# Optimization experiments

Hardware: AMD Instinct MI355X
Metric: run time of the kernel (lower is better)

Reference implementation:

```python
import jax, jax.numpy as jnp
import numpy as np

EPS = 1e-8

def prelu(x, a):
    return jnp.where(x >= 0, x, a * x)

def setup_inputs() -> dict:
    key = jax.random.key(0)
    ks = jax.random.split(key, 8)
    B, G, N, T = 4, 8, 128, 6000
    H = 384
    x = jax.random.normal(ks[0], (B, G, N, T), dtype=jnp.float32)
    # torch.nn.Linear default init: U(-1/sqrt(fan_in), 1/sqrt(fan_in))
    def lin(k, out_f, in_f):
        k1, k2 = jax.random.split(k)
        bound = 1.0 / np.sqrt(in_f)
        W = jax.random.uniform(k1, (out_f, in_f), minval=-bound, maxval=bound, dtype=jnp.float32)
        b = jax.random.uniform(k2, (out_f,), minval=-bound, maxval=bound, dtype=jnp.float32)
        return W, b
    Wi, bi = lin(ks[1], H, N)
    Wm, bm = lin(ks[2], H, H)
    Wo, bo = lin(ks[3], N, 2 * H)
    # PReLU default: single learnable scalar initialized to 0.25
    ai = jnp.float32(0.25)
    am = jnp.float32(0.25)
    ao = jnp.float32(0.25)
    gamma = jnp.ones((N,), dtype=jnp.float32)
    beta = jnp.zeros((N,), dtype=jnp.float32)
    return {"input": x, "Wi": Wi, "bi": bi, "ai": ai, "Wm": Wm, "bm": bm, "am": am,
            "Wo": Wo, "bo": bo, "ao": ao, "gamma": gamma, "beta": beta}

def reference(input, Wi, bi, ai, Wm, bm, am, Wo, bo, ao, gamma, beta):
    B, G, N, T = input.shape
    # [B, T, G, N]
    h = jnp.transpose(input, (0, 3, 1, 2))
    # TAC_input: Linear(N->H) + PReLU
    gi = prelu(jnp.einsum('btgn,hn->btgh', h, Wi) + bi, ai)          # [B,T,G,H]
    # mean over groups, TAC_mean: Linear(H->H) + PReLU
    gm = gi.mean(axis=2)                                              # [B,T,H]
    gm = prelu(jnp.einsum('bth,oh->bto', gm, Wm) + bm, am)            # [B,T,H]
    gm = jnp.broadcast_to(gm[:, :, None, :], gi.shape)                # [B,T,G,H]
    cat = jnp.concatenate([gi, gm], axis=-1)                          # [B,T,G,2H]
    # TAC_output: Linear(2H->N) + PReLU
    go = prelu(jnp.einsum('btgc,nc->btgn', cat, Wo) + bo, ao)         # [B,T,G,N]
    go = jnp.transpose(go, (0, 2, 3, 1))                              # [B,G,N,T]
    # GlobLN over (N, T) per (batch*G) sample, affine along channel N
    mean = go.mean(axis=(2, 3), keepdims=True)
    var = jnp.mean((go - mean) ** 2, axis=(2, 3), keepdims=True)
    normed = (go - mean) / jnp.sqrt(var + EPS)
    go = gamma[None, None, :, None] * normed + beta[None, None, :, None]
    return input + go
```

## Files before the change

kernel.cpp:

```cpp
#include <hip/hip_runtime.h>

typedef __bf16 bf16_t;
typedef __bf16 bf16x8 __attribute__((ext_vector_type(8)));
typedef float f32x4 __attribute__((ext_vector_type(4)));

static constexpr int Bq = 4, Gg = 8, Nn = 128, Tt = 6000, Hh = 384;
static constexpr int TB = 16;
static constexpr int NTPB = Tt / TB;
static constexpr int NTILES = Bq * NTPB;
static constexpr int LDA = 136;
static constexpr int LDG = 392;
static constexpr int LDSM = 392;
static constexpr int LDV = 132;

static constexpr size_t OFF_WI  = 0;
static constexpr size_t OFF_WM  = OFF_WI + (size_t)Hh * Nn * 2;
static constexpr size_t OFF_WO  = OFF_WM + (size_t)Hh * Hh * 2;
static constexpr size_t OFF_PT  = OFF_WO + (size_t)Nn * 2 * Hh * 2;
static constexpr size_t OFF_MRS = OFF_PT + (size_t)NTILES * 8 * 16 * 4;
static constexpr size_t OFF_GO  = (size_t)2 << 20;
static constexpr size_t WS_NEED = OFF_GO + (size_t)Bq * Tt * Gg * Nn * 2;

static constexpr int SM_GI = 0;
static constexpr int SM_SM = 100352;
static constexpr int SM_AS = 112896;
static constexpr int SM_MM = 112896;
static constexpr int SM_VV = 112896 + 12544;
static constexpr int SMEM_BYTES = 147712;

#define MFMA16(a, b, c) __builtin_amdgcn_mfma_f32_16x16x32_bf16((a), (b), (c), 0, 0, 0)

__global__ void k0_prep(const float* __restrict__ Wi, const float* __restrict__ Wm,
                        const float* __restrict__ Wo,
                        bf16_t* __restrict__ WiB, bf16_t* __restrict__ WmB,
                        bf16_t* __restrict__ WoB) {
    int i = blockIdx.x * blockDim.x + threadIdx.x;
    const int n1 = Hh * Nn, n2 = Hh * Hh, n3 = Nn * 2 * Hh;
    for (int idx = i; idx < n1 + n2 + n3; idx += gridDim.x * blockDim.x) {
        if (idx < n1)            WiB[idx] = (bf16_t)Wi[idx];
        else if (idx < n1 + n2)  WmB[idx - n1] = (bf16_t)Wm[idx - n1];
        else                     WoB[idx - n1 - n2] = (bf16_t)Wo[idx - n1 - n2];
    }
}

__device__ __forceinline__ int as_col(int row, int c) {
    return ((((c >> 3) ^ ((row >> 3) & 7)) << 3) | (c & 7));
}

__global__ __launch_bounds__(512, 1)
void k1_fused(const float* __restrict__ x,
              const bf16_t* __restrict__ WiB, const float* __restrict__ bi, const float* __restrict__ aip,
              const bf16_t* __restrict__ WmB, const float* __restrict__ bm, const float* __restrict__ amp,
              const bf16_t* __restrict__ WoB, const float* __restrict__ bo, const float* __restrict__ aop,
              bf16_t* __restrict__ go, float* __restrict__ part) {
    __shared__ char smem[SMEM_BYTES];
    bf16_t* Gi = (bf16_t*)(smem + SM_GI);
    bf16_t* Sm = (bf16_t*)(smem + SM_SM);
    bf16_t* As = (bf16_t*)(smem + SM_AS);
    bf16_t* Mm = (bf16_t*)(smem + SM_MM);
    float*  Vv = (float*)(smem + SM_VV);

    const int tid  = threadIdx.x;
    const int lane = tid & 63;
    const int w    = tid >> 6;
    const int l15  = lane & 15;
    const int l4   = lane >> 4;
    const int tile = blockIdx.x;
    const int b    = tile / NTPB, t0 = (tile % NTPB) * TB;

    {
        const int g0 = tid >> 7, n0 = tid & 127;
        #pragma unroll
        for (int h = 0; h < 2; h++) {
            int gg = g0 + 4 * h;
            #pragma unroll
            for (int q = 0; q < 4; q++) {
                f32x4 xv = *(const f32x4*)&x[((size_t)((b * Gg + gg) * Nn + n0)) * Tt + t0 + 4 * q];
                #pragma unroll
                for (int e = 0; e < 4; e++) {
                    int row = (q * 4 + e) * Gg + gg;
                    As[row * LDA + as_col(row, n0)] = (bf16_t)xv[e];
                }
            }
        }
    }
    __syncthreads();

    const float ai = aip[0], am = amp[0], ao = aop[0];

    {
        const int cb = w * 48;
        f32x4 acc[8][3];
        #pragma unroll
        for (int mt = 0; mt < 8; mt++)
            #pragma unroll
            for (int nc = 0; nc < 3; nc++) acc[mt][nc] = f32x4{0.f, 0.f, 0.f, 0.f};
        #pragma unroll
        for (int kk = 0; kk < 4; kk++) {
            const int k0 = kk * 32 + l4 * 8;
            bf16x8 bb[3];
            #pragma unroll
            for (int nc = 0; nc < 3; nc++)
                bb[nc] = *(const bf16x8*)&WiB[(cb + nc * 16 + l15) * Nn + k0];
            #pragma unroll
            for (int mt = 0; mt < 8; mt++) {
                int row = mt * 16 + l15;
                bf16x8 a = *(const bf16x8*)&As[row * LDA + as_col(row, k0)];
                #pragma unroll
                for (int nc = 0; nc < 3; nc++) acc[mt][nc] = MFMA16(a, bb[nc], acc[mt][nc]);
            }
        }
        #pragma unroll
        for (int nc = 0; nc < 3; nc++) {
            int col = cb + nc * 16 + l15;
            float bv = bi[col];
            #pragma unroll
            for (int mt = 0; mt < 8; mt++) {
                float ms = 0.f;
                #pragma unroll
                for (int j = 0; j < 4; j++) {
                    int row = mt * 16 + l4 * 4 + j;
                    float v = acc[mt][nc][j] + bv;
                    v = v >= 0.f ? v : ai * v;
                    Gi[row * LDG + col] = (bf16_t)v;
                    ms += v;
                }
                ms += __shfl_xor(ms, 16, 64);
                if ((l4 & 1) == 0) {
                    int tl = mt * 2 + (l4 >> 1);
                    Sm[tl * LDSM + col] = (bf16_t)(0.125f * ms);
                }
            }
        }
    }
    __syncthreads();

    {
        const int cb2 = w * 48;
        f32x4 acc2[3];
        #pragma unroll
        for (int nc = 0; nc < 3; nc++) acc2[nc] = f32x4{0.f, 0.f, 0.f, 0.f};
        #pragma unroll
        for (int kk = 0; kk < 12; kk++) {
            const int k0 = kk * 32 + l4 * 8;
            bf16x8 a = *(const bf16x8*)&Sm[l15 * LDSM + k0];
            #pragma unroll
            for (int nc = 0; nc < 3; nc++) {
                bf16x8 bb = *(const bf16x8*)&WmB[(cb2 + nc * 16 + l15) * Hh + k0];
                acc2[nc] = MFMA16(a, bb, acc2[nc]);
            }
        }
        #pragma unroll
        for (int nc = 0; nc < 3; nc++) {
            int col = cb2 + nc * 16 + l15;
            float bv = bm[col];
            #pragma unroll
            for (int j = 0; j < 4; j++) {
                float v = acc2[nc][j] + bv;
                v = v >= 0.f ? v : am * v;
                Mm[(l4 * 4 + j) * LDSM + col] = (bf16_t)v;
            }
        }
    }
    __syncthreads();

    {
        const int nblk = w * 16;
        f32x4 acc3 = f32x4{0.f, 0.f, 0.f, 0.f};
        #pragma unroll
        for (int kk = 0; kk < 12; kk++) {
            const int k0 = kk * 32 + l4 * 8;
            bf16x8 a = *(const bf16x8*)&Mm[l15 * LDSM + k0];
            bf16x8 bb = *(const bf16x8*)&WoB[(nblk + l15) * 768 + 384 + k0];
            acc3 = MFMA16(a, bb, acc3);
        }
        #pragma unroll
        for (int j = 0; j < 4; j++) Vv[(l4 * 4 + j) * LDV + nblk + l15] = acc3[j];
    }

    const int mh = w >> 2, ws4 = w & 3;
    const int cb4 = ws4 * 32;
    f32x4 acc4[4][2];
    #pragma unroll
    for (int mt = 0; mt < 4; mt++)
        #pragma unroll
        for (int nc = 0; nc < 2; nc++) acc4[mt][nc] = f32x4{0.f, 0.f, 0.f, 0.f};
    #pragma unroll
    for (int kk = 0; kk < 12; kk++) {
        const int k0 = kk * 32 + l4 * 8;
        bf16x8 b0 = *(const bf16x8*)&WoB[(cb4 + l15) * 768 + k0];
        bf16x8 b1 = *(const bf16x8*)&WoB[(cb4 + 16 + l15) * 768 + k0];
        bf16x8 a[4];
        #pragma unroll
        for (int mt = 0; mt < 4; mt++)
            a[mt] = *(const bf16x8*)&Gi[(mh * 64 + mt * 16 + l15) * LDG + k0];
        #pragma unroll
        for (int mt = 0; mt < 4; mt++) {
            acc4[mt][0] = MFMA16(a[mt], b0, acc4[mt][0]);
            acc4[mt][1] = MFMA16(a[mt], b1, acc4[mt][1]);
        }
    }
    __syncthreads();

    {
        float gsum[4] = {0.f, 0.f, 0.f, 0.f};
        float gss[4]  = {0.f, 0.f, 0.f, 0.f};
        #pragma unroll
        for (int nc = 0; nc < 2; nc++) {
            int col = cb4 + nc * 16 + l15;
            float bv = bo[col];
            #pragma unroll
            for (int mt = 0; mt < 4; mt++) {
                #pragma unroll
                for (int j = 0; j < 4; j++) {
                    int row = mh * 64 + mt * 16 + l4 * 4 + j;
                    int tl = row >> 3;
                    int g = row & 7;
                    float v = acc4[mt][nc][j] + Vv[tl * LDV + col] + bv;
                    v = v >= 0.f ? v : ao * v;
                    go[((size_t)((b * Tt + t0 + tl) * Gg + g)) * Nn + col] = (bf16_t)v;
                    gsum[j] += v;
                    gss[j] += v * v;
                }
            }
        }
        #pragma unroll
        for (int j = 0; j < 4; j++) {
            float s = gsum[j], q = gss[j];
            #pragma unroll
            for (int off = 1; off < 16; off <<= 1) {
                s += __shfl_xor(s, off, 64);
                q += __shfl_xor(q, off, 64);
            }
            s += __shfl_xor(s, 32, 64);
            q += __shfl_xor(q, 32, 64);
            if (l15 == 0 && l4 < 2) {
                int g = l4 * 4 + j;
                part[((size_t)tile * 8 + w) * 16 + g * 2 + 0] = s;
                part[((size_t)tile * 8 + w) * 16 + g * 2 + 1] = q;
            }
        }
    }
}

__global__ __launch_bounds__(1024)
void k_final(const float* __restrict__ part, float* __restrict__ mr) {
    __shared__ float red[64][17];
    const int tid = threadIdx.x, key = tid & 63, chunk = tid >> 6;
    const int bb = key >> 4;
    const int rowsPerB = NTPB * 8;
    const int t0 = chunk * 188;
    const int cnt = min(188, rowsPerB - t0);
    float s = 0.f;
    for (int i = 0; i < cnt; i++)
        s += part[(size_t)(bb * rowsPerB + t0 + i) * 16 + (key & 15)];
    red[key][chunk] = s;
    __syncthreads();
    if (tid < 64) {
        float tot = 0.f;
        #pragma unroll
        for (int ch = 0; ch < 16; ch++) tot += red[tid][ch];
        red[tid][16] = tot;
    }
    __syncthreads();
    if (tid < 32) {
        int b2 = tid >> 3, g2 = tid & 7;
        float s0 = red[b2 * 16 + g2 * 2][16];
        float s1 = red[b2 * 16 + g2 * 2 + 1][16];
        const float cntf = (float)Nn * (float)Tt;
        float mean = s0 / cntf;
        float var = s1 / cntf - mean * mean;
        mr[tid * 2] = mean;
        mr[tid * 2 + 1] = rsqrtf(var + 1e-8f);
    }
}

__global__ __launch_bounds__(256)
void k_apply(const float* __restrict__ x, const bf16_t* __restrict__ go,
             const float* __restrict__ mr, const float* __restrict__ gamma,
             const float* __restrict__ beta, float* __restrict__ out) {
    __shared__ float tr[32][65];
    int bid = blockIdx.x;
    const int tt = bid % 94; bid /= 94;
    const int nn = bid & 3;  bid >>= 2;
    const int g = bid & 7;
    const int b = bid >> 3;
    const int t0 = tt * 64, n0 = nn * 32;
    const int tid = threadIdx.x;
    const float mean = mr[(b * 8 + g) * 2], rstd = mr[(b * 8 + g) * 2 + 1];

    for (int idx = tid; idx < 2048; idx += 256) {
        int nl = idx & 31, tl = idx >> 5;
        int t = t0 + tl;
        float v = 0.f;
        if (t < Tt) v = (float)go[((size_t)((b * Tt + t) * Gg + g)) * Nn + n0 + nl];
        tr[nl][tl] = v;
    }
    __syncthreads();
    for (int idx = tid; idx < 2048; idx += 256) {
        int tl = idx & 63, nl = idx >> 6;
        int t = t0 + tl;
        if (t < Tt) {
            int n = n0 + nl;
            size_t a = ((size_t)((b * Gg + g) * Nn + n)) * Tt + t;
            out[a] = x[a] + gamma[n] * (tr[nl][tl] - mean) * rstd + beta[n];
        }
    }
}

extern "C" void kernel_launch(void* const* d_in, const int* in_sizes, int n_in,
                              void* d_out, int out_size, void* d_ws, size_t ws_size,
                              hipStream_t stream) {
    const float* x     = (const float*)d_in[0];
    const float* Wi    = (const float*)d_in[1];
    const float* bi    = (const float*)d_in[2];
    const float* ai    = (const float*)d_in[3];
    const float* Wm    = (const float*)d_in[4];
    const float* bm    = (const float*)d_in[5];
    const float* am    = (const float*)d_in[6];
    const float* Wo    = (const float*)d_in[7];
    const float* bo    = (const float*)d_in[8];
    const float* ao    = (const float*)d_in[9];
    const float* gamma = (const float*)d_in[10];
    const float* beta  = (const float*)d_in[11];
    float* out = (float*)d_out;
    char* ws = (char*)d_ws;

    if (ws_size < WS_NEED) return;

    bf16_t* WiB = (bf16_t*)(ws + OFF_WI);
    bf16_t* WmB = (bf16_t*)(ws + OFF_WM);
    bf16_t* WoB = (bf16_t*)(ws + OFF_WO);
    float*  prt = (float*)(ws + OFF_PT);
    float*  mrs = (float*)(ws + OFF_MRS);
    bf16_t* goB = (bf16_t*)(ws + OFF_GO);

    k0_prep<<<dim3(512), dim3(256), 0, stream>>>(Wi, Wm, Wo, WiB, WmB, WoB);
    k1_fused<<<dim3(NTILES), dim3(512), 0, stream>>>(
        x, WiB, bi, ai, WmB, bm, am, WoB, bo, ao, goB, prt);
    k_final<<<dim3(1), dim3(1024), 0, stream>>>(prt, mrs);
    k_apply<<<dim3(Bq * Gg * 4 * 94), dim3(256), 0, stream>>>(x, goB, mrs, gamma, beta, out);
}
```

Before: 294.5 us.

## Stage biases in LDS, nontemporal I/O, per-tile stat reduction via shared atomics

```diff
diff --git a/kernel.cpp b/kernel.cpp
--- a/kernel.cpp
+++ b/kernel.cpp
@@ -17,7 +17,7 @@
 static constexpr size_t OFF_WM  = OFF_WI + (size_t)Hh * Nn * 2;
 static constexpr size_t OFF_WO  = OFF_WM + (size_t)Hh * Hh * 2;
 static constexpr size_t OFF_PT  = OFF_WO + (size_t)Nn * 2 * Hh * 2;
-static constexpr size_t OFF_MRS = OFF_PT + (size_t)NTILES * 8 * 16 * 4;
+static constexpr size_t OFF_MRS = OFF_PT + (size_t)NTILES * 16 * 4;
 static constexpr size_t OFF_GO  = (size_t)2 << 20;
 static constexpr size_t WS_NEED = OFF_GO + (size_t)Bq * Tt * Gg * Nn * 2;
 
@@ -26,7 +26,11 @@
 static constexpr int SM_AS = 112896;
 static constexpr int SM_MM = 112896;
 static constexpr int SM_VV = 112896 + 12544;
-static constexpr int SMEM_BYTES = 147712;
+static constexpr int SM_BI = 147712;
+static constexpr int SM_BM = 149248;
+static constexpr int SM_BO = 150784;
+static constexpr int SM_ST = 151296;
+static constexpr int SMEM_BYTES = 151360;
 
 #define MFMA16(a, b, c) __builtin_amdgcn_mfma_f32_16x16x32_bf16((a), (b), (c), 0, 0, 0)
 
@@ -59,6 +63,10 @@
     bf16_t* As = (bf16_t*)(smem + SM_AS);
     bf16_t* Mm = (bf16_t*)(smem + SM_MM);
     float*  Vv = (float*)(smem + SM_VV);
+    float*  sbi = (float*)(smem + SM_BI);
+    float*  sbm = (float*)(smem + SM_BM);
+    float*  sbo = (float*)(smem + SM_BO);
+    float*  st  = (float*)(smem + SM_ST);
 
     const int tid  = threadIdx.x;
     const int lane = tid & 63;
@@ -68,6 +76,10 @@
     const int tile = blockIdx.x;
     const int b    = tile / NTPB, t0 = (tile % NTPB) * TB;
 
+    if (tid < 384) { sbi[tid] = bi[tid]; sbm[tid] = bm[tid]; }
+    if (tid >= 384 && tid < 512) sbo[tid - 384] = bo[tid - 384];
+    if (tid < 16) st[tid] = 0.f;
+
     {
         const int g0 = tid >> 7, n0 = tid & 127;
         #pragma unroll
@@ -75,7 +87,8 @@
             int gg = g0 + 4 * h;
             #pragma unroll
             for (int q = 0; q < 4; q++) {
-                f32x4 xv = *(const f32x4*)&x[((size_t)((b * Gg + gg) * Nn + n0)) * Tt + t0 + 4 * q];
+                f32x4 xv = __builtin_nontemporal_load(
+                    (const f32x4*)&x[((size_t)((b * Gg + gg) * Nn + n0)) * Tt + t0 + 4 * q]);
                 #pragma unroll
                 for (int e = 0; e < 4; e++) {
                     int row = (q * 4 + e) * Gg + gg;
@@ -113,7 +126,7 @@
         #pragma unroll
         for (int nc = 0; nc < 3; nc++) {
             int col = cb + nc * 16 + l15;
-            float bv = bi[col];
+            float bv = sbi[col];
             #pragma unroll
             for (int mt = 0; mt < 8; mt++) {
                 float ms = 0.f;
@@ -153,7 +166,7 @@
         #pragma unroll
         for (int nc = 0; nc < 3; nc++) {
             int col = cb2 + nc * 16 + l15;
-            float bv = bm[col];
+            float bv = sbm[col];
             #pragma unroll
             for (int j = 0; j < 4; j++) {
                 float v = acc2[nc][j] + bv;
@@ -208,7 +221,7 @@
         #pragma unroll
         for (int nc = 0; nc < 2; nc++) {
             int col = cb4 + nc * 16 + l15;
-            float bv = bo[col];
+            float bv = sbo[col];
             #pragma unroll
             for (int mt = 0; mt < 4; mt++) {
                 #pragma unroll
@@ -218,7 +231,8 @@
                     int g = row & 7;
                     float v = acc4[mt][nc][j] + Vv[tl * LDV + col] + bv;
                     v = v >= 0.f ? v : ao * v;
-                    go[((size_t)((b * Tt + t0 + tl) * Gg + g)) * Nn + col] = (bf16_t)v;
+                    __builtin_nontemporal_store(
+                        (bf16_t)v, &go[((size_t)((b * Tt + t0 + tl) * Gg + g)) * Nn + col]);
                     gsum[j] += v;
                     gss[j] += v * v;
                 }
@@ -236,37 +250,40 @@
             q += __shfl_xor(q, 32, 64);
             if (l15 == 0 && l4 < 2) {
                 int g = l4 * 4 + j;
-                part[((size_t)tile * 8 + w) * 16 + g * 2 + 0] = s;
-                part[((size_t)tile * 8 + w) * 16 + g * 2 + 1] = q;
-            }
-        }
-    }
+                atomicAdd(&st[g * 2 + 0], s);
+                atomicAdd(&st[g * 2 + 1], q);
+            }
+        }
+    }
+    __syncthreads();
+    if (tid < 16) part[(size_t)tile * 16 + tid] = st[tid];
 }
 
 __global__ __launch_bounds__(1024)
 void k_final(const float* __restrict__ part, float* __restrict__ mr) {
-    __shared__ float red[64][17];
-    const int tid = threadIdx.x, key = tid & 63, chunk = tid >> 6;
-    const int bb = key >> 4;
-    const int rowsPerB = NTPB * 8;
-    const int t0 = chunk * 188;
-    const int cnt = min(188, rowsPerB - t0);
-    float s = 0.f;
-    for (int i = 0; i < cnt; i++)
-        s += part[(size_t)(bb * rowsPerB + t0 + i) * 16 + (key & 15)];
-    red[key][chunk] = s;
-    __syncthreads();
-    if (tid < 64) {
-        float tot = 0.f;
-        #pragma unroll
-        for (int ch = 0; ch < 16; ch++) tot += red[tid][ch];
-        red[tid][16] = tot;
-    }
-    __syncthreads();
+    __shared__ float red[64][16];
+    __shared__ float tot[4][16];
+    const int tid = threadIdx.x;
+    const int col = tid & 15, rb = tid >> 4;
+    float s[4] = {0.f, 0.f, 0.f, 0.f};
+    for (int k = 0; k < 24; k++) {
+        int row = rb + (k << 6);
+        if (row < NTILES) s[row / NTPB] += part[(size_t)row * 16 + col];
+    }
+    for (int b2 = 0; b2 < 4; b2++) {
+        red[rb][col] = s[b2];
+        __syncthreads();
+        if (tid < 16) {
+            float t = 0.f;
+            #pragma unroll 8
+            for (int r = 0; r < 64; r++) t += red[r][tid];
+            tot[b2][tid] = t;
+        }
+        __syncthreads();
+    }
     if (tid < 32) {
         int b2 = tid >> 3, g2 = tid & 7;
-        float s0 = red[b2 * 16 + g2 * 2][16];
-        float s1 = red[b2 * 16 + g2 * 2 + 1][16];
+        float s0 = tot[b2][g2 * 2], s1 = tot[b2][g2 * 2 + 1];
         const float cntf = (float)Nn * (float)Tt;
         float mean = s0 / cntf;
         float var = s1 / cntf - mean * mean;
```

After: 297.3 us. About the same (+0.9%).
